# Performance work log

Hardware: AMD Instinct MI355X
Metric: run time of the kernel (lower is better)

## Reference

```python
import jax, jax.numpy as jnp
import numpy as np

N = 50000      # num_nodes
E = 800000     # num_edges
F_IN = 128     # node_features
H = 128        # hidden_channels
EPS = 1e-5     # BatchNorm eps


def setup_inputs() -> dict:
    key = jax.random.key(0)
    ks = jax.random.split(key, 6)
    x = jax.random.normal(ks[0], (N, F_IN), dtype=jnp.float32)
    edge_index = jax.random.randint(ks[1], (2, E), 0, N, dtype=jnp.int64)
    s = 0.05
    return {
        "x": x,
        "edge_index": edge_index,
        "g_in": jnp.ones((F_IN,), jnp.float32),
        "be_in": jnp.zeros((F_IN,), jnp.float32),
        "w1": jax.random.normal(ks[2], (F_IN, 2 * H), jnp.float32) * s,
        "b1": jnp.zeros((2 * H,), jnp.float32),
        "g1": jnp.ones((2 * H,), jnp.float32),
        "be1": jnp.zeros((2 * H,), jnp.float32),
        "w2": jax.random.normal(ks[3], (2 * H, H), jnp.float32) * s,
        "b2": jnp.zeros((H,), jnp.float32),
        "g2": jnp.ones((H,), jnp.float32),
        "be2": jnp.zeros((H,), jnp.float32),
    }


def batchnorm(x, g, b):
    # training-mode BatchNorm1d: batch stats over the node dimension (biased var)
    m = jnp.mean(x, axis=0)
    v = jnp.var(x, axis=0)
    return (x - m) * jax.lax.rsqrt(v + EPS) * g + b


def gcn_conv(x, w, b, src, dst, deg_inv_sqrt):
    # PyG GCNConv: transform, then D^{-1/2}(A+I)D^{-1/2} aggregation, then bias
    h = x @ w                                   # [N, out]
    norm = deg_inv_sqrt[src] * deg_inv_sqrt[dst]  # [E+N]
    msg = h[src] * norm[:, None]                # gather + scale
    out = jax.ops.segment_sum(msg, dst, num_segments=N)  # scatter-add
    return out + b


def reference(x, edge_index, g_in, be_in, w1, b1, g1, be1, w2, b2, g2, be2):
    # add self-loops once
    loop = jnp.arange(N, dtype=edge_index.dtype)
    src = jnp.concatenate([edge_index[0], loop])
    dst = jnp.concatenate([edge_index[1], loop])
    deg = jax.ops.segment_sum(jnp.ones_like(src, dtype=x.dtype), dst, num_segments=N)
    deg_inv_sqrt = jnp.where(deg > 0, jax.lax.rsqrt(jnp.maximum(deg, 1.0)), 0.0)

    h = batchnorm(x, g_in, be_in)
    # layer 1: F_IN -> 2H (no residual: shapes differ); dropout is identity in eval
    h = jax.nn.relu(batchnorm(gcn_conv(h, w1, b1, src, dst, deg_inv_sqrt), g1, be1))
    # layer 2 (final): 2H -> H
    h = jax.nn.relu(batchnorm(gcn_conv(h, w2, b2, src, dst, deg_inv_sqrt), g2, be2))
    return h
```

## Files before the change

kernel.cpp:

```cpp
#include <hip/hip_runtime.h>
#include <hip/hip_bf16.h>

#define NN 50000
#define NE 800000
#define FIN 128
#define HC1 256
#define HC2 128
#define EPSV 1e-5f
#define SLOT 64

typedef __attribute__((ext_vector_type(8))) short bf8;
typedef __attribute__((ext_vector_type(16))) float f32x16;

union BF8U { bf8 v; ushort u[8]; uint4 q; };

__device__ __forceinline__ float bf2f(ushort u) {
    union { uint i; float f; } c; c.i = ((uint)u) << 16; return c.f;
}
__device__ __forceinline__ ushort f2bf(float f) {
    return __builtin_bit_cast(ushort, __float2bfloat16(f));
}

__global__ void k_init(int* __restrict__ cnt, float* __restrict__ stats) {
    int i = blockIdx.x * blockDim.x + threadIdx.x;
    if (i < NN) cnt[i] = 0;
    if (i < 1024) stats[i] = 0.0f;
}

#define CB 3125
#define SB 391
#define WB 128

__device__ __forceinline__ void wprep_body(const float* __restrict__ W, ushort* __restrict__ wp,
                                           int idx, int K, int NC) {
    int j = idx & 7;
    int lane = (idx >> 3) & 63;
    int ts = idx >> 9;
    int KS = K / 16;
    int s = ts % KS;
    int t = ts / KS;
    int n = t * 32 + (lane & 31);
    int k = s * 16 + (lane >> 5) * 8 + j;
    wp[idx] = f2bf(W[(size_t)k * NC + n]);
}

__global__ __launch_bounds__(256) void k_pre(
    const int* __restrict__ ei, int* __restrict__ cnt, int* __restrict__ slots,
    const float* __restrict__ x, float* __restrict__ sum, float* __restrict__ sumsq,
    const float* __restrict__ w1, ushort* __restrict__ wp1,
    const float* __restrict__ w2, ushort* __restrict__ wp2) {
    int b = blockIdx.x;
    int t = threadIdx.x;
    if (b < CB) {
        int e = b * 256 + t;
        if (e < NE) {
            int s = ei[e];
            int d = ei[NE + e];
            s = min(max(s, 0), NN - 1);
            d = min(max(d, 0), NN - 1);
            int pos = atomicAdd(&cnt[d], 1);
            if (pos < SLOT) slots[(size_t)d * SLOT + pos] = s;
        }
        return;
    }
    if (b < CB + SB) {
        const int F4 = 32, RIF = 8, RPB = 128;
        int c4 = t & 31;
        int ro = t >> 5;
        int r0 = (b - CB) * RPB;
        int r1 = min(r0 + RPB, NN);
        float4 s = make_float4(0.f, 0.f, 0.f, 0.f);
        float4 q = make_float4(0.f, 0.f, 0.f, 0.f);
        for (int r = r0 + ro; r < r1; r += RIF) {
            float4 v = ((const float4*)x)[(size_t)r * F4 + c4];
            s.x += v.x; s.y += v.y; s.z += v.z; s.w += v.w;
            q.x += v.x * v.x; q.y += v.y * v.y; q.z += v.z * v.z; q.w += v.w * v.w;
        }
        __shared__ float4 sS[256];
        __shared__ float4 sQ[256];
        sS[t] = s; sQ[t] = q;
        __syncthreads();
#pragma unroll
        for (int st = 128; st >= 32; st >>= 1) {
            if (t < st) {
                float4 a = sS[t + st], bb = sQ[t + st];
                sS[t].x += a.x; sS[t].y += a.y; sS[t].z += a.z; sS[t].w += a.w;
                sQ[t].x += bb.x; sQ[t].y += bb.y; sQ[t].z += bb.z; sQ[t].w += bb.w;
            }
            __syncthreads();
        }
        if (t < 32) {
            float4 a = sS[t], bb = sQ[t];
            atomicAdd(&sum[t * 4 + 0], a.x); atomicAdd(&sum[t * 4 + 1], a.y);
            atomicAdd(&sum[t * 4 + 2], a.z); atomicAdd(&sum[t * 4 + 3], a.w);
            atomicAdd(&sumsq[t * 4 + 0], bb.x); atomicAdd(&sumsq[t * 4 + 1], bb.y);
            atomicAdd(&sumsq[t * 4 + 2], bb.z); atomicAdd(&sumsq[t * 4 + 3], bb.w);
        }
        return;
    }
    if (b < CB + SB + WB) {
        wprep_body(w1, wp1, (b - CB - SB) * 256 + t, FIN, HC1);
        return;
    }
    wprep_body(w2, wp2, (b - CB - SB - WB) * 256 + t, HC1, HC2);
}

template<int C>
__global__ void k_finalize(const float* __restrict__ sum, const float* __restrict__ sumsq,
                           const float* __restrict__ g, const float* __restrict__ be,
                           float* __restrict__ scale, float* __restrict__ shift) {
    int c = threadIdx.x;
    if (c < C) {
        float mean = sum[c] / (float)NN;
        float var = sumsq[c] / (float)NN - mean * mean;
        var = fmaxf(var, 0.f);
        float sc = g[c] * rsqrtf(var + EPSV);
        scale[c] = sc;
        shift[c] = be[c] - mean * sc;
    }
}

__global__ void k_s0(const float* __restrict__ x, const int* __restrict__ cnt,
                     const float* __restrict__ scale, const float* __restrict__ shift,
                     ushort* __restrict__ s0) {
    int idx = blockIdx.x * blockDim.x + threadIdx.x;
    const int total = NN * FIN / 4;
    if (idx >= total) return;
    int row = idx >> 5;
    int c4 = idx & 31;
    float4 v = ((const float4*)x)[idx];
    float4 sc = ((const float4*)scale)[c4];
    float4 sh = ((const float4*)shift)[c4];
    float d = rsqrtf((float)(cnt[row] + 1));
    ushort4 o;
    o.x = f2bf((v.x * sc.x + sh.x) * d);
    o.y = f2bf((v.y * sc.y + sh.y) * d);
    o.z = f2bf((v.z * sc.z + sh.z) * d);
    o.w = f2bf((v.w * sc.w + sh.w) * d);
    ((ushort4*)s0)[idx] = o;
}

__global__ __launch_bounds__(256) void k_gather(
    const int* __restrict__ cnt, const int* __restrict__ slots,
    const ushort* __restrict__ src, ushort* __restrict__ agg) {
    int w = threadIdx.x >> 6;
    int lane = threadIdx.x & 63;
    int r = blockIdx.x * 4 + w;
    if (r >= NN) return;
    int degR = cnt[r];
    int deg = min(degR, SLOT);
    int half = lane >> 5;
    int l5 = lane & 31;
    const uint2* sp = (const uint2*)src;
    const int* sl = slots + (size_t)r * SLOT;
    float a0 = 0.f, a1 = 0.f, a2 = 0.f, a3 = 0.f;
    if (half == 0) {
        uint2 v = sp[(size_t)r * 32 + l5];
        a0 += bf2f((ushort)(v.x & 0xffffu)); a1 += bf2f((ushort)(v.x >> 16));
        a2 += bf2f((ushort)(v.y & 0xffffu)); a3 += bf2f((ushort)(v.y >> 16));
    }
    int j = half;
    for (; j + 6 < deg; j += 8) {
        int s0 = sl[j], s1 = sl[j + 2], s2 = sl[j + 4], s3 = sl[j + 6];
        uint2 v0 = sp[(size_t)s0 * 32 + l5];
        uint2 v1 = sp[(size_t)s1 * 32 + l5];
        uint2 v2 = sp[(size_t)s2 * 32 + l5];
        uint2 v3 = sp[(size_t)s3 * 32 + l5];
        a0 += (bf2f((ushort)(v0.x & 0xffffu)) + bf2f((ushort)(v1.x & 0xffffu)))
            + (bf2f((ushort)(v2.x & 0xffffu)) + bf2f((ushort)(v3.x & 0xffffu)));
        a1 += (bf2f((ushort)(v0.x >> 16)) + bf2f((ushort)(v1.x >> 16)))
            + (bf2f((ushort)(v2.x >> 16)) + bf2f((ushort)(v3.x >> 16)));
        a2 += (bf2f((ushort)(v0.y & 0xffffu)) + bf2f((ushort)(v1.y & 0xffffu)))
            + (bf2f((ushort)(v2.y & 0xffffu)) + bf2f((ushort)(v3.y & 0xffffu)));
        a3 += (bf2f((ushort)(v0.y >> 16)) + bf2f((ushort)(v1.y >> 16)))
            + (bf2f((ushort)(v2.y >> 16)) + bf2f((ushort)(v3.y >> 16)));
    }
    for (; j < deg; j += 2) {
        int s = sl[j];
        uint2 v = sp[(size_t)s * 32 + l5];
        a0 += bf2f((ushort)(v.x & 0xffffu)); a1 += bf2f((ushort)(v.x >> 16));
        a2 += bf2f((ushort)(v.y & 0xffffu)); a3 += bf2f((ushort)(v.y >> 16));
    }
    a0 += __shfl_xor(a0, 32, 64);
    a1 += __shfl_xor(a1, 32, 64);
    a2 += __shfl_xor(a2, 32, 64);
    a3 += __shfl_xor(a3, 32, 64);
    if (half == 0) {
        float d = rsqrtf((float)(degR + 1));
        uint2 o;
        o.x = ((uint)f2bf(a1 * d) << 16) | (uint)f2bf(a0 * d);
        o.y = ((uint)f2bf(a3 * d) << 16) | (uint)f2bf(a2 * d);
        ((uint2*)agg)[(size_t)r * 32 + l5] = o;
    }
}

__global__ __launch_bounds__(256) void k_mm1(
    const ushort* __restrict__ Abf,
    const ushort* __restrict__ wp,
    const float* __restrict__ bias,
    ushort* __restrict__ Y,
    float* __restrict__ sum, float* __restrict__ sumsq)
{
    const int K = 128, NC = 256, KS = K / 16, NT = NC / 32;
    int tid = threadIdx.x;
    int wid = tid >> 6;
    int lane = tid & 63;
    int rbase = blockIdx.x * 128 + wid * 32;
    int arow = rbase + (lane & 31);
    int khalf = lane >> 5;

    __shared__ float lsum[NC];
    __shared__ float lsq[NC];
    lsum[tid] = 0.f; lsq[tid] = 0.f;
    __syncthreads();

    f32x16 acc[NT];
#pragma unroll
    for (int t = 0; t < NT; ++t)
#pragma unroll
        for (int i = 0; i < 16; ++i) acc[t][i] = 0.f;

    const uint4* Bq = (const uint4*)wp;
    const uint4* Aq = (const uint4*)Abf;
#pragma unroll
    for (int s = 0; s < KS; ++s) {
        BF8U au;
        if (arow < NN) au.q = Aq[(size_t)arow * (K / 8) + s * 2 + khalf];
        else au.q = make_uint4(0, 0, 0, 0);
#pragma unroll
        for (int t = 0; t < NT; ++t) {
            BF8U bu;
            bu.q = Bq[(t * KS + s) * 64 + lane];
            acc[t] = __builtin_amdgcn_mfma_f32_32x32x16_bf16(au.v, bu.v, acc[t], 0, 0, 0);
        }
    }

#pragma unroll
    for (int t = 0; t < NT; ++t) {
        int col = t * 32 + (lane & 31);
        float bv = bias[col];
        float fs = 0.f, fq = 0.f;
#pragma unroll
        for (int q = 0; q < 4; ++q) {
#pragma unroll
            for (int i = 0; i < 4; ++i) {
                int r = rbase + q * 8 + khalf * 4 + i;
                if (r < NN) {
                    float v = acc[t][q * 4 + i] + bv;
                    Y[(size_t)r * NC + col] = f2bf(v);
                    fs += v; fq += v * v;
                }
            }
        }
        atomicAdd(&lsum[col], fs);
        atomicAdd(&lsq[col], fq);
    }
    __syncthreads();
    atomicAdd(&sum[tid], lsum[tid]);
    atomicAdd(&sumsq[tid], lsq[tid]);
}

__global__ __launch_bounds__(256) void k_mm2(
    const ushort* __restrict__ Y,
    const ushort* __restrict__ wp,
    const float* __restrict__ sc,
    const float* __restrict__ sh,
    const int* __restrict__ cnt,
    ushort* __restrict__ S2)
{
    const int K = 256, NC = 128, KS = K / 16, NT = NC / 32;
    int wid = threadIdx.x >> 6;
    int lane = threadIdx.x & 63;
    int rbase = blockIdx.x * 128 + wid * 32;
    int arow = rbase + (lane & 31);
    int khalf = lane >> 5;

    f32x16 acc[NT];
#pragma unroll
    for (int t = 0; t < NT; ++t)
#pragma unroll
        for (int i = 0; i < 16; ++i) acc[t][i] = 0.f;

    const uint4* Bq = (const uint4*)wp;
#pragma unroll
    for (int s = 0; s < KS; ++s) {
        int k0 = s * 16 + khalf * 8;
        BF8U au;
        if (arow < NN) {
            uint4 y = *(const uint4*)&Y[(size_t)arow * K + k0];
            float4 c0 = *(const float4*)&sc[k0];
            float4 c1 = *(const float4*)&sc[k0 + 4];
            float4 h0 = *(const float4*)&sh[k0];
            float4 h1 = *(const float4*)&sh[k0 + 4];
            au.u[0] = f2bf(fmaxf(bf2f((ushort)(y.x & 0xffffu)) * c0.x + h0.x, 0.f));
            au.u[1] = f2bf(fmaxf(bf2f((ushort)(y.x >> 16))     * c0.y + h0.y, 0.f));
            au.u[2] = f2bf(fmaxf(bf2f((ushort)(y.y & 0xffffu)) * c0.z + h0.z, 0.f));
            au.u[3] = f2bf(fmaxf(bf2f((ushort)(y.y >> 16))     * c0.w + h0.w, 0.f));
            au.u[4] = f2bf(fmaxf(bf2f((ushort)(y.z & 0xffffu)) * c1.x + h1.x, 0.f));
            au.u[5] = f2bf(fmaxf(bf2f((ushort)(y.z >> 16))     * c1.y + h1.y, 0.f));
            au.u[6] = f2bf(fmaxf(bf2f((ushort)(y.w & 0xffffu)) * c1.z + h1.z, 0.f));
            au.u[7] = f2bf(fmaxf(bf2f((ushort)(y.w >> 16))     * c1.w + h1.w, 0.f));
        } else {
            au.q = make_uint4(0, 0, 0, 0);
        }
#pragma unroll
        for (int t = 0; t < NT; ++t) {
            BF8U bu;
            bu.q = Bq[(t * KS + s) * 64 + lane];
            acc[t] = __builtin_amdgcn_mfma_f32_32x32x16_bf16(au.v, bu.v, acc[t], 0, 0, 0);
        }
    }

#pragma unroll
    for (int q = 0; q < 4; ++q) {
#pragma unroll
        for (int i = 0; i < 4; ++i) {
            int r = rbase + q * 8 + khalf * 4 + i;
            if (r < NN) {
                float dv = rsqrtf((float)(cnt[r] + 1));
#pragma unroll
                for (int t = 0; t < NT; ++t) {
                    int col = t * 32 + (lane & 31);
                    S2[(size_t)r * NC + col] = f2bf(acc[t][q * 4 + i] * dv);
                }
            }
        }
    }
}

__global__ __launch_bounds__(256) void k_post2(const ushort* __restrict__ agg2,
                                               const float* __restrict__ b2,
                                               float* __restrict__ sum, float* __restrict__ sumsq) {
    const int F4 = 32, RIF = 8, RPB = 128;
    int t = threadIdx.x;
    int c4 = t & 31;
    int ro = t >> 5;
    int r0 = blockIdx.x * RPB;
    int r1 = min(r0 + RPB, NN);
    float4 bb = ((const float4*)b2)[c4];
    float4 s = make_float4(0.f, 0.f, 0.f, 0.f);
    float4 q = make_float4(0.f, 0.f, 0.f, 0.f);
    for (int r = r0 + ro; r < r1; r += RIF) {
        ushort4 u = ((const ushort4*)agg2)[(size_t)r * F4 + c4];
        float4 v;
        v.x = bf2f(u.x) + bb.x; v.y = bf2f(u.y) + bb.y;
        v.z = bf2f(u.z) + bb.z; v.w = bf2f(u.w) + bb.w;
        s.x += v.x; s.y += v.y; s.z += v.z; s.w += v.w;
        q.x += v.x * v.x; q.y += v.y * v.y; q.z += v.z * v.z; q.w += v.w * v.w;
    }
    __shared__ float4 sS[256];
    __shared__ float4 sQ[256];
    sS[t] = s; sQ[t] = q;
    __syncthreads();
#pragma unroll
    for (int st = 128; st >= F4; st >>= 1) {
        if (t < st) {
            float4 a = sS[t + st], b = sQ[t + st];
            sS[t].x += a.x; sS[t].y += a.y; sS[t].z += a.z; sS[t].w += a.w;
            sQ[t].x += b.x; sQ[t].y += b.y; sQ[t].z += b.z; sQ[t].w += b.w;
        }
        __syncthreads();
    }
    if (t < F4) {
        float4 a = sS[t], b = sQ[t];
        atomicAdd(&sum[t * 4 + 0], a.x); atomicAdd(&sum[t * 4 + 1], a.y);
        atomicAdd(&sum[t * 4 + 2], a.z); atomicAdd(&sum[t * 4 + 3], a.w);
        atomicAdd(&sumsq[t * 4 + 0], b.x); atomicAdd(&sumsq[t * 4 + 1], b.y);
        atomicAdd(&sumsq[t * 4 + 2], b.z); atomicAdd(&sumsq[t * 4 + 3], b.w);
    }
}

__global__ void k_bnrelu(const ushort* __restrict__ agg2, const float* __restrict__ b2,
                         const float* __restrict__ scale, const float* __restrict__ shift,
                         float* __restrict__ out) {
    int idx = blockIdx.x * blockDim.x + threadIdx.x;
    const int total = NN * HC2 / 4;
    if (idx >= total) return;
    int c4 = idx & 31;
    float4 sc = ((const float4*)scale)[c4];
    float4 sh = ((const float4*)shift)[c4];
    float4 bb = ((const float4*)b2)[c4];
    ushort4 u = ((const ushort4*)agg2)[idx];
    float4 v;
    v.x = fmaxf((bf2f(u.x) + bb.x) * sc.x + sh.x, 0.f);
    v.y = fmaxf((bf2f(u.y) + bb.y) * sc.y + sh.y, 0.f);
    v.z = fmaxf((bf2f(u.z) + bb.z) * sc.z + sh.z, 0.f);
    v.w = fmaxf((bf2f(u.w) + bb.w) * sc.w + sh.w, 0.f);
    ((float4*)out)[idx] = v;
}

extern "C" void kernel_launch(void* const* d_in, const int* in_sizes, int n_in,
                              void* d_out, int out_size, void* d_ws, size_t ws_size,
                              hipStream_t stream) {
    const float* x     = (const float*)d_in[0];
    const int*   ei    = (const int*)d_in[1];
    const float* g_in  = (const float*)d_in[2];
    const float* be_in = (const float*)d_in[3];
    const float* w1    = (const float*)d_in[4];
    const float* b1    = (const float*)d_in[5];
    const float* g1    = (const float*)d_in[6];
    const float* be1   = (const float*)d_in[7];
    const float* w2    = (const float*)d_in[8];
    const float* b2    = (const float*)d_in[9];
    const float* g2    = (const float*)d_in[10];
    const float* be2   = (const float*)d_in[11];
    float* out = (float*)d_out;

    float* ws = (float*)d_ws;
    float* stats = ws;
    float* sumIn = stats;        float* sqIn = stats + 128;
    float* sum1  = stats + 256;  float* sq1  = stats + 512;
    float* sum2  = stats + 768;  float* sq2  = stats + 896;
    float* params = ws + 1024;
    float* scIn = params;        float* shIn = params + 128;
    float* sc1  = params + 256;  float* sh1  = params + 512;
    float* sc2  = params + 768;  float* sh2  = params + 896;
    ushort* wp1   = (ushort*)(ws + 2048);
    ushort* wp2   = (ushort*)(ws + 18432);
    ushort* y1u   = (ushort*)(ws + 34816);
    ushort* s0bf  = (ushort*)(ws + 6434816);
    ushort* aggbf = (ushort*)(ws + 9634816);
    int* cnt   = (int*)(ws + 12834816);
    int* slots = (int*)(ws + 12884816);

    const int sblocks = (NN + 127) / 128;

    hipLaunchKernelGGL(k_init, dim3((NN + 255) / 256), dim3(256), 0, stream, cnt, stats);

    hipLaunchKernelGGL(k_pre, dim3(CB + SB + 2 * WB), dim3(256), 0, stream,
                       ei, cnt, slots, x, sumIn, sqIn, w1, wp1, w2, wp2);

    hipLaunchKernelGGL(k_finalize<128>, dim3(1), dim3(128), 0, stream,
                       sumIn, sqIn, g_in, be_in, scIn, shIn);

    hipLaunchKernelGGL(k_s0, dim3((NN * 32 + 255) / 256), dim3(256), 0, stream,
                       x, cnt, scIn, shIn, s0bf);

    hipLaunchKernelGGL(k_gather, dim3((NN + 3) / 4), dim3(256), 0, stream,
                       cnt, slots, s0bf, aggbf);

    hipLaunchKernelGGL(k_mm1, dim3(sblocks), dim3(256), 0, stream, aggbf, wp1, b1, y1u, sum1, sq1);
    hipLaunchKernelGGL(k_finalize<256>, dim3(1), dim3(256), 0, stream, sum1, sq1, g1, be1, sc1, sh1);

    hipLaunchKernelGGL(k_mm2, dim3(sblocks), dim3(256), 0, stream, y1u, wp2, sc1, sh1, cnt, s0bf);
    hipLaunchKernelGGL(k_gather, dim3((NN + 3) / 4), dim3(256), 0, stream,
                       cnt, slots, s0bf, aggbf);

    hipLaunchKernelGGL(k_post2, dim3(sblocks), dim3(256), 0, stream, aggbf, b2, sum2, sq2);
    hipLaunchKernelGGL(k_finalize<128>, dim3(1), dim3(128), 0, stream, sum2, sq2, g2, be2, sc2, sh2);
    hipLaunchKernelGGL(k_bnrelu, dim3((NN * 32 + 255) / 256), dim3(256), 0, stream,
                       aggbf, b2, sc2, sh2, out);
}
```

Measured before the change: 284.3 us.

## Build compact padded CSR via tile bucketing instead of per-node atomic slot lists

Replaces the per-destination global atomic slot array with a two-pass build. Edges are first bucketed into 256-node tiles using shared-memory histograms, then each tile is sorted into a compact CSR of 16-bit source ids padded to multiples of 16, with a zero sentinel row. The gather kernel now reads 16 ids per vector load and does full-wave 64-lane row loads with no half-wave reduction, and the input BN finalize is folded into the CSR kernel. This cuts global atomic contention and index traffic, but per-tile capacity caps could silently drop edges on skewed graphs.

After: 247.3 us. 13.0% less time.

```diff
diff --git a/kernel.cpp b/kernel.cpp
--- a/kernel.cpp
+++ b/kernel.cpp
@@ -7,7 +7,9 @@
 #define HC1 256
 #define HC2 128
 #define EPSV 1e-5f
-#define SLOT 64
+#define NTILE 196
+#define CAP 8448
+#define FILLMAX (CAP - 3840)
 
 typedef __attribute__((ext_vector_type(8))) short bf8;
 typedef __attribute__((ext_vector_type(16))) float f32x16;
@@ -17,17 +19,24 @@
 __device__ __forceinline__ float bf2f(ushort u) {
     union { uint i; float f; } c; c.i = ((uint)u) << 16; return c.f;
 }
+__device__ __forceinline__ float ulo(uint u) {
+    union { uint i; float f; } c; c.i = u << 16; return c.f;
+}
+__device__ __forceinline__ float uhi(uint u) {
+    union { uint i; float f; } c; c.i = u & 0xffff0000u; return c.f;
+}
 __device__ __forceinline__ ushort f2bf(float f) {
     return __builtin_bit_cast(ushort, __float2bfloat16(f));
 }
 
-__global__ void k_init(int* __restrict__ cnt, float* __restrict__ stats) {
+__global__ void k_init(int* __restrict__ gcur, float* __restrict__ stats, uint* __restrict__ s0row) {
     int i = blockIdx.x * blockDim.x + threadIdx.x;
-    if (i < NN) cnt[i] = 0;
+    if (i < 256) gcur[i] = 0;
     if (i < 1024) stats[i] = 0.0f;
-}
-
-#define CB 3125
+    if (i < 64) s0row[i] = 0u;
+}
+
+#define BKB NTILE
 #define SB 391
 #define WB 128
 
@@ -44,30 +53,53 @@
     wp[idx] = f2bf(W[(size_t)k * NC + n]);
 }
 
-__global__ __launch_bounds__(256) void k_pre(
-    const int* __restrict__ ei, int* __restrict__ cnt, int* __restrict__ slots,
+__global__ __launch_bounds__(256) void k_bucket(
+    const int* __restrict__ ei, int* __restrict__ gcur, uint* __restrict__ buckets,
     const float* __restrict__ x, float* __restrict__ sum, float* __restrict__ sumsq,
     const float* __restrict__ w1, ushort* __restrict__ wp1,
     const float* __restrict__ w2, ushort* __restrict__ wp2) {
     int b = blockIdx.x;
     int t = threadIdx.x;
-    if (b < CB) {
-        int e = b * 256 + t;
-        if (e < NE) {
-            int s = ei[e];
-            int d = ei[NE + e];
-            s = min(max(s, 0), NN - 1);
-            d = min(max(d, 0), NN - 1);
-            int pos = atomicAdd(&cnt[d], 1);
-            if (pos < SLOT) slots[(size_t)d * SLOT + pos] = s;
+    if (b < BKB) {
+        __shared__ int hist[NTILE];
+        __shared__ int base[NTILE];
+        if (t < NTILE) hist[t] = 0;
+        __syncthreads();
+        int e0 = b * 4096;
+        int es[16], ed[16];
+#pragma unroll
+        for (int i = 0; i < 16; ++i) {
+            int e = e0 + i * 256 + t;
+            if (e < NE) {
+                int s = ei[e];
+                int d = ei[NE + e];
+                s = min(max(s, 0), NN - 1);
+                d = min(max(d, 0), NN - 1);
+                es[i] = s; ed[i] = d;
+                atomicAdd(&hist[d >> 8], 1);
+            } else es[i] = -1;
+        }
+        __syncthreads();
+        if (t < NTILE) base[t] = atomicAdd(&gcur[t], hist[t]);
+        __syncthreads();
+        if (t < NTILE) hist[t] = 0;
+        __syncthreads();
+#pragma unroll
+        for (int i = 0; i < 16; ++i) {
+            if (es[i] >= 0) {
+                int tile = ed[i] >> 8;
+                int lofs = atomicAdd(&hist[tile], 1);
+                int pos = base[tile] + lofs;
+                if (pos < CAP) buckets[(size_t)tile * CAP + pos] = ((uint)es[i] << 8) | (uint)(ed[i] & 255);
+            }
         }
         return;
     }
-    if (b < CB + SB) {
+    if (b < BKB + SB) {
         const int F4 = 32, RIF = 8, RPB = 128;
         int c4 = t & 31;
         int ro = t >> 5;
-        int r0 = (b - CB) * RPB;
+        int r0 = (b - BKB) * RPB;
         int r1 = min(r0 + RPB, NN);
         float4 s = make_float4(0.f, 0.f, 0.f, 0.f);
         float4 q = make_float4(0.f, 0.f, 0.f, 0.f);
@@ -98,25 +130,79 @@
         }
         return;
     }
-    if (b < CB + SB + WB) {
-        wprep_body(w1, wp1, (b - CB - SB) * 256 + t, FIN, HC1);
+    if (b < BKB + SB + WB) {
+        wprep_body(w1, wp1, (b - BKB - SB) * 256 + t, FIN, HC1);
         return;
     }
-    wprep_body(w2, wp2, (b - CB - SB - WB) * 256 + t, HC1, HC2);
-}
-
-template<int C>
-__global__ void k_finalize(const float* __restrict__ sum, const float* __restrict__ sumsq,
-                           const float* __restrict__ g, const float* __restrict__ be,
-                           float* __restrict__ scale, float* __restrict__ shift) {
-    int c = threadIdx.x;
-    if (c < C) {
-        float mean = sum[c] / (float)NN;
-        float var = sumsq[c] / (float)NN - mean * mean;
-        var = fmaxf(var, 0.f);
-        float sc = g[c] * rsqrtf(var + EPSV);
-        scale[c] = sc;
-        shift[c] = be[c] - mean * sc;
+    wprep_body(w2, wp2, (b - BKB - SB - WB) * 256 + t, HC1, HC2);
+}
+
+__global__ __launch_bounds__(256) void k_csr(
+    const int* __restrict__ gcur, const uint* __restrict__ buckets,
+    ushort* __restrict__ csr, int* __restrict__ cnt, int* __restrict__ rowstart,
+    const float* __restrict__ sum, const float* __restrict__ sumsq,
+    const float* __restrict__ g, const float* __restrict__ be,
+    float* __restrict__ scale, float* __restrict__ shift) {
+    int t = threadIdx.x;
+    if (blockIdx.x == NTILE) {
+        if (t < 128) {
+            float mean = sum[t] / (float)NN;
+            float var = sumsq[t] / (float)NN - mean * mean;
+            var = fmaxf(var, 0.f);
+            float sc = g[t] * rsqrtf(var + EPSV);
+            scale[t] = sc;
+            shift[t] = be[t] - mean * sc;
+        }
+        return;
+    }
+    __shared__ uint ubuf[CAP];
+    __shared__ int cnt256[256];
+    __shared__ int scan[256];
+    __shared__ int offs256[256];
+    __shared__ int cur256[256];
+    int tile = blockIdx.x;
+    int t0 = tile << 8;
+    int size = min(gcur[tile], FILLMAX);
+    cnt256[t] = 0;
+    __syncthreads();
+    for (int i = t; i < size; i += 256) {
+        uint u = buckets[(size_t)tile * CAP + i];
+        ubuf[i] = u;
+        atomicAdd(&cnt256[u & 255u], 1);
+    }
+    __syncthreads();
+    int c = cnt256[t];
+    int padded = (c + 15) & ~15;
+    scan[t] = padded;
+    __syncthreads();
+#pragma unroll
+    for (int off = 1; off < 256; off <<= 1) {
+        int v = (t >= off) ? scan[t - off] : 0;
+        __syncthreads();
+        scan[t] += v;
+        __syncthreads();
+    }
+    int excl = scan[t] - padded;
+    offs256[t] = excl;
+    cur256[t] = 0;
+    int r = t0 + t;
+    if (r < NN) {
+        cnt[r] = c;
+        rowstart[r] = tile * CAP + excl;
+    }
+    __syncthreads();
+    for (int i = t; i < size; i += 256) {
+        uint u = ubuf[i];
+        int l = u & 255u;
+        int p = atomicAdd(&cur256[l], 1);
+        int w = offs256[l] + p;
+        if (w < CAP) csr[(size_t)tile * CAP + w] = (ushort)(u >> 8);
+    }
+    if (r < NN) {
+        for (int p = c; p < padded; ++p) {
+            int w = excl + p;
+            if (w < CAP) csr[(size_t)tile * CAP + w] = (ushort)NN;
+        }
     }
 }
 
@@ -141,57 +227,43 @@
 }
 
 __global__ __launch_bounds__(256) void k_gather(
-    const int* __restrict__ cnt, const int* __restrict__ slots,
-    const ushort* __restrict__ src, ushort* __restrict__ agg) {
-    int w = threadIdx.x >> 6;
+    const int* __restrict__ cnt, const int* __restrict__ rowstart,
+    const ushort* __restrict__ csr, const ushort* __restrict__ src,
+    ushort* __restrict__ agg) {
+    int wid = threadIdx.x >> 6;
     int lane = threadIdx.x & 63;
-    int r = blockIdx.x * 4 + w;
+    int r = blockIdx.x * 4 + wid;
     if (r >= NN) return;
-    int degR = cnt[r];
-    int deg = min(degR, SLOT);
-    int half = lane >> 5;
-    int l5 = lane & 31;
-    const uint2* sp = (const uint2*)src;
-    const int* sl = slots + (size_t)r * SLOT;
-    float a0 = 0.f, a1 = 0.f, a2 = 0.f, a3 = 0.f;
-    if (half == 0) {
-        uint2 v = sp[(size_t)r * 32 + l5];
-        a0 += bf2f((ushort)(v.x & 0xffffu)); a1 += bf2f((ushort)(v.x >> 16));
-        a2 += bf2f((ushort)(v.y & 0xffffu)); a3 += bf2f((ushort)(v.y >> 16));
-    }
-    int j = half;
-    for (; j + 6 < deg; j += 8) {
-        int s0 = sl[j], s1 = sl[j + 2], s2 = sl[j + 4], s3 = sl[j + 6];
-        uint2 v0 = sp[(size_t)s0 * 32 + l5];
-        uint2 v1 = sp[(size_t)s1 * 32 + l5];
-        uint2 v2 = sp[(size_t)s2 * 32 + l5];
-        uint2 v3 = sp[(size_t)s3 * 32 + l5];
-        a0 += (bf2f((ushort)(v0.x & 0xffffu)) + bf2f((ushort)(v1.x & 0xffffu)))
-            + (bf2f((ushort)(v2.x & 0xffffu)) + bf2f((ushort)(v3.x & 0xffffu)));
-        a1 += (bf2f((ushort)(v0.x >> 16)) + bf2f((ushort)(v1.x >> 16)))
-            + (bf2f((ushort)(v2.x >> 16)) + bf2f((ushort)(v3.x >> 16)));
-        a2 += (bf2f((ushort)(v0.y & 0xffffu)) + bf2f((ushort)(v1.y & 0xffffu)))
-            + (bf2f((ushort)(v2.y & 0xffffu)) + bf2f((ushort)(v3.y & 0xffffu)));
-        a3 += (bf2f((ushort)(v0.y >> 16)) + bf2f((ushort)(v1.y >> 16)))
-            + (bf2f((ushort)(v2.y >> 16)) + bf2f((ushort)(v3.y >> 16)));
-    }
-    for (; j < deg; j += 2) {
-        int s = sl[j];
-        uint2 v = sp[(size_t)s * 32 + l5];
-        a0 += bf2f((ushort)(v.x & 0xffffu)); a1 += bf2f((ushort)(v.x >> 16));
-        a2 += bf2f((ushort)(v.y & 0xffffu)); a3 += bf2f((ushort)(v.y >> 16));
-    }
-    a0 += __shfl_xor(a0, 32, 64);
-    a1 += __shfl_xor(a1, 32, 64);
-    a2 += __shfl_xor(a2, 32, 64);
-    a3 += __shfl_xor(a3, 32, 64);
-    if (half == 0) {
-        float d = rsqrtf((float)(degR + 1));
-        uint2 o;
-        o.x = ((uint)f2bf(a1 * d) << 16) | (uint)f2bf(a0 * d);
-        o.y = ((uint)f2bf(a3 * d) << 16) | (uint)f2bf(a2 * d);
-        ((uint2*)agg)[(size_t)r * 32 + l5] = o;
-    }
+    int deg = cnt[r];
+    int padded = (deg + 15) & ~15;
+    int base = rowstart[r];
+    const uint* sp = (const uint*)src;
+    uint v = sp[(size_t)r * 64 + lane];
+    float a0 = ulo(v), a1 = uhi(v);
+    for (int j = 0; j < padded; j += 16) {
+        const ushort* p = csr + base + j;
+        uint4 q0 = *(const uint4*)p;
+        uint4 q1 = *(const uint4*)(p + 8);
+        uint id[16];
+        id[0]  = q0.x & 0xffffu; id[1]  = q0.x >> 16;
+        id[2]  = q0.y & 0xffffu; id[3]  = q0.y >> 16;
+        id[4]  = q0.z & 0xffffu; id[5]  = q0.z >> 16;
+        id[6]  = q0.w & 0xffffu; id[7]  = q0.w >> 16;
+        id[8]  = q1.x & 0xffffu; id[9]  = q1.x >> 16;
+        id[10] = q1.y & 0xffffu; id[11] = q1.y >> 16;
+        id[12] = q1.z & 0xffffu; id[13] = q1.z >> 16;
+        id[14] = q1.w & 0xffffu; id[15] = q1.w >> 16;
+#pragma unroll
+        for (int k = 0; k < 16; ++k) id[k] = min(id[k], (uint)NN);
+        uint vv[16];
+#pragma unroll
+        for (int k = 0; k < 16; ++k) vv[k] = sp[(size_t)id[k] * 64 + lane];
+#pragma unroll
+        for (int k = 0; k < 16; ++k) { a0 += ulo(vv[k]); a1 += uhi(vv[k]); }
+    }
+    float d = rsqrtf((float)(deg + 1));
+    uint o = ((uint)f2bf(a1 * d) << 16) | (uint)f2bf(a0 * d);
+    ((uint*)agg)[(size_t)r * 64 + lane] = o;
 }
 
 __global__ __launch_bounds__(256) void k_mm1(
@@ -258,6 +330,21 @@
     __syncthreads();
     atomicAdd(&sum[tid], lsum[tid]);
     atomicAdd(&sumsq[tid], lsq[tid]);
+}
+
+template<int C>
+__global__ void k_finalize(const float* __restrict__ sum, const float* __restrict__ sumsq,
+                           const float* __restrict__ g, const float* __restrict__ be,
+                           float* __restrict__ scale, float* __restrict__ shift) {
+    int c = threadIdx.x;
+    if (c < C) {
+        float mean = sum[c] / (float)NN;
+        float var = sumsq[c] / (float)NN - mean * mean;
+        var = fmaxf(var, 0.f);
+        float sc = g[c] * rsqrtf(var + EPSV);
+        scale[c] = sc;
+        shift[c] = be[c] - mean * sc;
+    }
 }
 
 __global__ __launch_bounds__(256) void k_mm2(
@@ -419,32 +506,37 @@
     ushort* wp2   = (ushort*)(ws + 18432);
     ushort* y1u   = (ushort*)(ws + 34816);
     ushort* s0bf  = (ushort*)(ws + 6434816);
-    ushort* aggbf = (ushort*)(ws + 9634816);
-    int* cnt   = (int*)(ws + 12834816);
-    int* slots = (int*)(ws + 12884816);
+    ushort* aggbf = (ushort*)(ws + 9634880);
+    int* cnt      = (int*)(ws + 12834880);
+    int* rowstart = (int*)(ws + 12884880);
+    int* gcur     = (int*)(ws + 12934880);
+    uint* buckets = (uint*)(ws + 12935136);
+    ushort* csr   = (ushort*)(ws + 14590944);
 
     const int sblocks = (NN + 127) / 128;
 
-    hipLaunchKernelGGL(k_init, dim3((NN + 255) / 256), dim3(256), 0, stream, cnt, stats);
-
-    hipLaunchKernelGGL(k_pre, dim3(CB + SB + 2 * WB), dim3(256), 0, stream,
-                       ei, cnt, slots, x, sumIn, sqIn, w1, wp1, w2, wp2);
-
-    hipLaunchKernelGGL(k_finalize<128>, dim3(1), dim3(128), 0, stream,
+    hipLaunchKernelGGL(k_init, dim3(4), dim3(256), 0, stream,
+                       gcur, stats, (uint*)s0bf + (size_t)NN * 64);
+
+    hipLaunchKernelGGL(k_bucket, dim3(BKB + SB + 2 * WB), dim3(256), 0, stream,
+                       ei, gcur, buckets, x, sumIn, sqIn, w1, wp1, w2, wp2);
+
+    hipLaunchKernelGGL(k_csr, dim3(NTILE + 1), dim3(256), 0, stream,
+                       gcur, buckets, csr, cnt, rowstart,
                        sumIn, sqIn, g_in, be_in, scIn, shIn);
 
     hipLaunchKernelGGL(k_s0, dim3((NN * 32 + 255) / 256), dim3(256), 0, stream,
                        x, cnt, scIn, shIn, s0bf);
 
     hipLaunchKernelGGL(k_gather, dim3((NN + 3) / 4), dim3(256), 0, stream,
-                       cnt, slots, s0bf, aggbf);
+                       cnt, rowstart, csr, s0bf, aggbf);
 
     hipLaunchKernelGGL(k_mm1, dim3(sblocks), dim3(256), 0, stream, aggbf, wp1, b1, y1u, sum1, sq1);
     hipLaunchKernelGGL(k_finalize<256>, dim3(1), dim3(256), 0, stream, sum1, sq1, g1, be1, sc1, sh1);
 
     hipLaunchKernelGGL(k_mm2, dim3(sblocks), dim3(256), 0, stream, y1u, wp2, sc1, sh1, cnt, s0bf);
     hipLaunchKernelGGL(k_gather, dim3((NN + 3) / 4), dim3(256), 0, stream,
-                       cnt, slots, s0bf, aggbf);
+                       cnt, rowstart, csr, s0bf, aggbf);
 
     hipLaunchKernelGGL(k_post2, dim3(sblocks), dim3(256), 0, stream, aggbf, b2, sum2, sq2);
     hipLaunchKernelGGL(k_finalize<128>, dim3(1), dim3(128), 0, stream, sum2, sq2, g2, be2, sc2, sh2);
```
